# Performance work log

Measured on AMD Instinct MI355X. Metric: run time of the kernel, lower is better.

The kernel has to match this reference:

```python
import jax, jax.numpy as jnp
import numpy as np

B, T, D = 32, 512, 512
MAX_DUR = 8               # durations drawn from [0, MAX_DUR)
MAX_FRAMES = T * (MAX_DUR - 1)  # 3584 -> static upper bound on expanded length; pad to it
MAX_FRAMES = 4096          # round up to a nice static size


def setup_inputs() -> dict:
    key = jax.random.key(0)
    kx, kd = jax.random.split(key)
    x = jax.random.normal(kx, (B, T, D), dtype=jnp.float32)
    durations = jax.random.randint(kd, (B, T), 0, MAX_DUR, dtype=jnp.int32)
    return {"x": x, "durations": durations}


def reference(x, durations):
    # x: [B, T, D] float, durations: [B, T] int
    # Expansion via cumsum offsets + searchsorted gather (fused equivalent of
    # the host loop of repeat/cat/pad in the torch module).
    ends = jnp.cumsum(durations, axis=1)          # [B, T] exclusive end offsets
    total = ends[:, -1]                            # [B] true expanded lengths
    pos = jnp.arange(MAX_FRAMES, dtype=ends.dtype) # [F]
    # frame p belongs to token t where starts[t] <= p < ends[t]
    idx = jax.vmap(lambda e: jnp.searchsorted(e, pos, side='right'))(ends)  # [B, F]
    idx = jnp.clip(idx, 0, x.shape[1] - 1)
    out = jnp.take_along_axis(x, idx[:, :, None], axis=1)  # [B, F, D]
    mask = pos[None, :] < total[:, None]                    # [B, F]
    out = out * mask[:, :, None].astype(out.dtype)          # zero-pad beyond mel_len
    # torch fallback: an all-zero-duration row yields one zero frame, len 1
    mel_lens = jnp.maximum(total, 1).astype(jnp.int32)
    return out, mel_lens
```

## Files before the change

kernel.cpp:

```cpp
#include <hip/hip_runtime.h>

#define B_ 32
#define T_ 512
#define D_ 512
#define MAXF_ 4096

typedef float f4 __attribute__((ext_vector_type(4)));

__global__ __launch_bounds__(512) void lr_prep_kernel(const int* __restrict__ dur,
                                                      int* __restrict__ idx_map,
                                                      float* __restrict__ mel_out) {
    __shared__ int wsum[8];
    const int b = blockIdx.x;
    const int t = threadIdx.x;
    const int lane = t & 63;
    const int wave = t >> 6;
    const int d = dur[b * T_ + t];
    int v = d;
    #pragma unroll
    for (int off = 1; off < 64; off <<= 1) {
        int u = __shfl_up(v, off, 64);
        if (lane >= off) v += u;
    }
    if (lane == 63) wsum[wave] = v;
    __syncthreads();
    int woff = 0, total = 0;
    #pragma unroll
    for (int w = 0; w < 8; ++w) {
        const int s = wsum[w];
        woff  += (w < wave) ? s : 0;
        total += s;
    }
    const int end = v + woff;
    const int start = end - d;
    if (t == 0) mel_out[b] = (float)(total > 1 ? total : 1);
    int* __restrict__ im = idx_map + b * MAXF_;
    for (int p = start; p < end; ++p) im[p] = t;
    for (int p = total + t; p < MAXF_; p += T_) im[p] = -1;
}

#define FPB_ 16
__global__ __launch_bounds__(256) void lr_gather_kernel(const f4* __restrict__ x,
                                                        const int* __restrict__ idx_map,
                                                        f4* __restrict__ out) {
    __shared__ int s_idx[FPB_];
    const int tid = threadIdx.x;
    const int bid = ((blockIdx.x & 7) << 10) + (blockIdx.x >> 3);
    const int f0 = bid * FPB_;
    if (tid < FPB_) s_idx[tid] = idx_map[f0 + tid];
    __syncthreads();
    const int b = bid >> 8;
    const f4* __restrict__ xb = x + ((size_t)(b * T_) << 7);
    const int c = tid & 127;
    const size_t base = ((size_t)f0 << 7) + tid;
    #pragma unroll
    for (int k = 0; k < 8; ++k) {
        const int fl = (tid >> 7) + 2 * k;
        const int idx = s_idx[fl];
        const int cidx = idx < 0 ? 0 : idx;
        f4 v = xb[((size_t)cidx << 7) + c];
        if (idx < 0) v = (f4){0.f, 0.f, 0.f, 0.f};
        out[base + (size_t)k * 256] = v;
    }
}

extern "C" void kernel_launch(void* const* d_in, const int* in_sizes, int n_in,
                              void* d_out, int out_size, void* d_ws, size_t ws_size,
                              hipStream_t stream) {
    const float* x = (const float*)d_in[0];
    const int* durations = (const int*)d_in[1];
    float* out = (float*)d_out;
    float* mel_out = out + (size_t)B_ * MAXF_ * D_;
    int* idx_map = (int*)d_ws;

    lr_prep_kernel<<<B_, T_, 0, stream>>>(durations, idx_map, mel_out);

    const size_t n_vec4 = (size_t)B_ * MAXF_ * (D_ / 4);
    lr_gather_kernel<<<(int)(n_vec4 / (FPB_ * (D_ / 4))), 256, 0, stream>>>(
        (const f4*)x, idx_map, (f4*)out);
}
```

Before: 292.8 us.

## Fuse duration prefix-scan into gather kernel, recomputing index map per block

Merges the prep and gather kernels into one launch. Each block recomputes the per-batch prefix sum of durations (two tokens per thread) and builds its own 32-frame index map in shared memory, so no global index map is written or read. Frames per block also go from 16 to 32 to spread out the redundant scan. The cost is that every block repeats the 512-element scan.

```diff
diff --git a/kernel.cpp b/kernel.cpp
--- a/kernel.cpp
+++ b/kernel.cpp
@@ -4,63 +4,69 @@
 #define T_ 512
 #define D_ 512
 #define MAXF_ 4096
+#define FPB_ 32
+#define NBLK_ (B_ * MAXF_ / FPB_)
+#define CPB_ (MAXF_ / FPB_)
 
 typedef float f4 __attribute__((ext_vector_type(4)));
 
-__global__ __launch_bounds__(512) void lr_prep_kernel(const int* __restrict__ dur,
-                                                      int* __restrict__ idx_map,
-                                                      float* __restrict__ mel_out) {
-    __shared__ int wsum[8];
-    const int b = blockIdx.x;
-    const int t = threadIdx.x;
-    const int lane = t & 63;
-    const int wave = t >> 6;
-    const int d = dur[b * T_ + t];
-    int v = d;
+__global__ __launch_bounds__(256) void lr_fused_kernel(const f4* __restrict__ x,
+                                                       const int* __restrict__ dur,
+                                                       f4* __restrict__ out,
+                                                       float* __restrict__ mel_out) {
+    __shared__ int wsum[4];
+    __shared__ int im[FPB_];
+    const int tid = threadIdx.x;
+    const int bid = ((blockIdx.x & 7) << 9) + (blockIdx.x >> 3);
+    const int b  = bid >> 7;
+    const int f0 = (bid & 127) * FPB_;
+
+    const int2 d2 = ((const int2*)(dur + b * T_))[tid];
+    const int dsum = d2.x + d2.y;
+    const int lane = tid & 63;
+    const int wave = tid >> 6;
+    int v = dsum;
     #pragma unroll
     for (int off = 1; off < 64; off <<= 1) {
         int u = __shfl_up(v, off, 64);
         if (lane >= off) v += u;
     }
     if (lane == 63) wsum[wave] = v;
+    if (tid < FPB_) im[tid] = -1;
     __syncthreads();
     int woff = 0, total = 0;
     #pragma unroll
-    for (int w = 0; w < 8; ++w) {
+    for (int w = 0; w < 4; ++w) {
         const int s = wsum[w];
         woff  += (w < wave) ? s : 0;
         total += s;
     }
-    const int end = v + woff;
-    const int start = end - d;
-    if (t == 0) mel_out[b] = (float)(total > 1 ? total : 1);
-    int* __restrict__ im = idx_map + b * MAXF_;
-    for (int p = start; p < end; ++p) im[p] = t;
-    for (int p = total + t; p < MAXF_; p += T_) im[p] = -1;
-}
+    const int excl = woff + v - dsum;
 
-#define FPB_ 16
-__global__ __launch_bounds__(256) void lr_gather_kernel(const f4* __restrict__ x,
-                                                        const int* __restrict__ idx_map,
-                                                        f4* __restrict__ out) {
-    __shared__ int s_idx[FPB_];
-    const int tid = threadIdx.x;
-    const int bid = ((blockIdx.x & 7) << 10) + (blockIdx.x >> 3);
-    const int f0 = bid * FPB_;
-    if (tid < FPB_) s_idx[tid] = idx_map[f0 + tid];
+    const int f1 = f0 + FPB_;
+    {
+        const int s0 = excl, e0 = excl + d2.x;
+        const int lo = s0 > f0 ? s0 : f0, hi = e0 < f1 ? e0 : f1;
+        for (int p = lo; p < hi; ++p) im[p - f0] = 2 * tid;
+        const int e1 = e0 + d2.y;
+        const int lo1 = e0 > f0 ? e0 : f0, hi1 = e1 < f1 ? e1 : f1;
+        for (int p = lo1; p < hi1; ++p) im[p - f0] = 2 * tid + 1;
+    }
+    if ((bid & 127) == 0 && tid == 0)
+        mel_out[b] = (float)(total > 1 ? total : 1);
     __syncthreads();
-    const int b = bid >> 8;
+
     const f4* __restrict__ xb = x + ((size_t)(b * T_) << 7);
     const int c = tid & 127;
-    const size_t base = ((size_t)f0 << 7) + tid;
+    const size_t base = (((size_t)b * MAXF_ + f0) << 7) + tid;
     #pragma unroll
-    for (int k = 0; k < 8; ++k) {
+    for (int k = 0; k < 16; ++k) {
         const int fl = (tid >> 7) + 2 * k;
-        const int idx = s_idx[fl];
+        const int idx = im[fl];
         const int cidx = idx < 0 ? 0 : idx;
-        f4 v = xb[((size_t)cidx << 7) + c];
-        if (idx < 0) v = (f4){0.f, 0.f, 0.f, 0.f};
-        out[base + (size_t)k * 256] = v;
+        f4 vv = xb[((size_t)cidx << 7) + c];
+        if (idx < 0) vv = (f4){0.f, 0.f, 0.f, 0.f};
+        out[base + (size_t)k * 256] = vv;
     }
 }
 
@@ -71,11 +77,8 @@
     const int* durations = (const int*)d_in[1];
     float* out = (float*)d_out;
     float* mel_out = out + (size_t)B_ * MAXF_ * D_;
-    int* idx_map = (int*)d_ws;
+    (void)d_ws; (void)ws_size;
 
-    lr_prep_kernel<<<B_, T_, 0, stream>>>(durations, idx_map, mel_out);
-
-    const size_t n_vec4 = (size_t)B_ * MAXF_ * (D_ / 4);
-    lr_gather_kernel<<<(int)(n_vec4 / (FPB_ * (D_ / 4))), 256, 0, stream>>>(
-        (const f4*)x, idx_map, (f4*)out);
+    lr_fused_kernel<<<NBLK_, 256, 0, stream>>>(
+        (const f4*)x, durations, (f4*)out, mel_out);
 }
```

Result: no change. 292.0 us (-0.3%).
